# Optimization experiments

Hardware: AMD Instinct MI355X
Metric: run time of the kernel (lower is better)

Reference implementation:

```python
import jax, jax.numpy as jnp
import numpy as np

N = 100000      # nodes
E = 3200000     # edges (avg degree 32)
DU = 256        # unary_channels
DP = 256        # pairwise_channels (== out_channels, required by fusion cat)
H = 64          # hidden_channels = out_channels // 4
DO = 256        # out_channels
STEPS = 1
EPS = 1e-5      # BatchNorm eps (torch default)


def _bn(h, gamma, beta):
    # BatchNorm1d, training-mode batch stats (biased variance, as torch normalizes)
    mu = jnp.mean(h, axis=0)
    var = jnp.var(h, axis=0)
    return gamma * (h - mu) * jax.lax.rsqrt(var + EPS) + beta


def setup_inputs() -> dict:
    key = jax.random.key(0)
    ks = jax.random.split(key, 12)
    edge_index = jax.random.randint(ks[0], (2, E), 0, N, dtype=jnp.int64)
    return {
        "x": jax.random.normal(ks[1], (N, DU), dtype=jnp.float32),
        "y": jax.random.normal(ks[2], (N, DP), dtype=jnp.float32),
        "pos": jax.random.normal(ks[3], (N, 3), dtype=jnp.float32),
        "edge_index": edge_index,
        "Wu": jax.random.normal(ks[4], (DU, H), dtype=jnp.float32) / np.sqrt(DU),
        "gu": jnp.ones((H,), jnp.float32), "bu": jnp.zeros((H,), jnp.float32),
        "Wp": jax.random.normal(ks[5], (DP, H), dtype=jnp.float32) / np.sqrt(DP),
        "gp": jnp.ones((H,), jnp.float32), "bp": jnp.zeros((H,), jnp.float32),
        "c": jnp.eye(H, dtype=jnp.float32) + 0.1 * jax.random.normal(ks[6], (H, H), dtype=jnp.float32),
        "Wm": jax.random.normal(ks[7], (H, DO), dtype=jnp.float32) / np.sqrt(H),
        "gm": jnp.ones((DO,), jnp.float32), "bm": jnp.zeros((DO,), jnp.float32),
        "Wf": jax.random.normal(ks[8], (2 * DO, DO), dtype=jnp.float32) / np.sqrt(2 * DO),
        "gf": jnp.ones((DO,), jnp.float32), "bf": jnp.zeros((DO,), jnp.float32),
    }


def reference(x, y, pos, edge_index, Wu, gu, bu, Wp, gp, bp, c, Wm, gm, bm, Wf, gf, bf):
    i, j = edge_index[0], edge_index[1]
    # unary / pairwise embeddings (Linear no-bias + BN)
    xu = _bn(x @ Wu, gu, bu)                      # [N, H]
    su = _bn(y @ Wp, gp, bp)                      # [N, H]
    # edge logits: -||s_i - s_j||^2, softmax grouped by destination i
    d = su[i] - su[j]                             # [E, H]
    logit = -jnp.sum(d * d, axis=1, keepdims=True)  # [E, 1]
    m = jax.ops.segment_max(logit, i, num_segments=N)
    ex = jnp.exp(logit - m[i])
    denom = jax.ops.segment_sum(ex, i, num_segments=N)
    s = ex / (denom[i] + 1e-16)                   # [E, 1] edge softmax weights
    # CRF mean-field iterations with linear solve
    z = xu
    C = c.T @ c                                   # [H, H]
    Minv = jnp.linalg.inv(jnp.eye(H, dtype=x.dtype) + C)
    h = xu
    for _ in range(STEPS):
        agg = jax.ops.segment_sum(s * h[j], i, num_segments=N)  # gather-scale-scatter
        h = (z + agg @ C) @ Minv
    # output heads
    h = jax.nn.leaky_relu(_bn(h @ Wm, gm, bm))
    out = jax.nn.leaky_relu(_bn(jnp.concatenate([h, y], axis=-1) @ Wf, gf, bf))
    return out
```

## Files before the change

### kernel.cpp

```cpp
#include <hip/hip_runtime.h>
#include <hip/hip_fp16.h>
#include <math.h>

typedef unsigned short u16;
typedef short s16x8 __attribute__((ext_vector_type(8)));
typedef unsigned short u16x8 __attribute__((ext_vector_type(8)));
typedef float f32x4 __attribute__((ext_vector_type(4)));

__device__ __forceinline__ float bf2f(u16 u) {
  unsigned x = ((unsigned)u) << 16;
  return __uint_as_float(x);
}
__device__ __forceinline__ u16 f2bf(float f) {
  unsigned x = __float_as_uint(f);
  unsigned r = x + 0x7FFFu + ((x >> 16) & 1u);
  return (u16)(r >> 16);
}

static const size_t OFF_MINV   = 0;
static const size_t OFF_AU     = 32ull * 1024;
static const size_t OFF_BUE    = 32ull * 1024 + 256;
static const size_t OFF_AP     = 32ull * 1024 + 512;
static const size_t OFF_APBE   = 32ull * 1024 + 768;
static const size_t OFF_AM     = 36ull * 1024;
static const size_t OFF_BM     = 37ull * 1024;
static const size_t OFF_AF     = 38ull * 1024;
static const size_t OFF_BF     = 39ull * 1024;
static const size_t OFF_BTOT   = 40ull * 1024;
static const size_t OFF_BOFF   = 44ull * 1024;
static const size_t OFF_WUT    = 64ull * 1024;
static const size_t OFF_WMT    = 128ull * 1024;
static const size_t OFF_WFT    = 192ull * 1024;
static const size_t OFF_WPH    = 512ull * 1024;
static const size_t OFF_WPL    = 576ull * 1024;
static const size_t OFF_PART1  = 1ull  * 1024 * 1024;
static const size_t OFF_PART2  = 2ull  * 1024 * 1024;
static const size_t OFF_ROWPTR = 3ull  * 1024 * 1024;
static const size_t OFF_BLKCNT = 5ull  * 1024 * 1024;
static const size_t OFF_SRCJ   = 18ull * 1024 * 1024;
static const size_t OFF_U      = 44ull * 1024 * 1024;
static const size_t OFF_UN     = 57ull * 1024 * 1024;
static const size_t OFF_P      = 70ull * 1024 * 1024;
static const size_t OFF_PS     = 109ull * 1024 * 1024;
static const size_t OFF_H2     = 122ull * 1024 * 1024;

#define NBLK_BIN 1024

__global__ __launch_bounds__(256) void k_prep(const float* __restrict__ c,
                                              float* __restrict__ minv_out) {
  __shared__ float CC[4096];
  __shared__ float aug[64 * 129];
  __shared__ float fs[64];
  float* cl = aug;
  int t = threadIdx.x;
  for (int idx = t; idx < 4096; idx += 256) cl[idx] = c[idx];
  __syncthreads();
  for (int idx = t; idx < 4096; idx += 256) {
    int a = idx >> 6, b = idx & 63;
    float s = (a == b) ? 1.f : 0.f;
    for (int k = 0; k < 64; ++k) s += cl[k * 64 + a] * cl[k * 64 + b];
    CC[idx] = s;
  }
  __syncthreads();
  for (int idx = t; idx < 8192; idx += 256) {
    int r = idx >> 7, cc = idx & 127;
    aug[r * 129 + cc] = (cc < 64) ? CC[r * 64 + cc] : (((cc - 64) == r) ? 1.f : 0.f);
  }
  __syncthreads();
  int cloc = t & 127;
  int rbase = t >> 7;
  for (int p = 0; p < 64; ++p) {
    float inv = 1.0f / aug[p * 129 + p];
    if (t < 64) fs[t] = (t == p) ? 0.f : aug[t * 129 + p];
    __syncthreads();
    if (t < 128) aug[p * 129 + t] *= inv;
    __syncthreads();
    float pc = aug[p * 129 + cloc];
#pragma unroll
    for (int rr = 0; rr < 64; rr += 2) {
      int r = rr + rbase;
      aug[r * 129 + cloc] -= fs[r] * pc;
    }
    __syncthreads();
  }
  for (int idx = t; idx < 4096; idx += 256) {
    int r = idx >> 6, cc = idx & 63;
    minv_out[idx] = aug[r * 129 + 64 + cc];
  }
}

__global__ __launch_bounds__(256) void k_tcvt(const float* __restrict__ in, u16* __restrict__ outb,
                                              int Kd, int Nc) {
  int i = blockIdx.x * 256 + threadIdx.x;
  if (i < Kd * Nc) {
    int k = i / Nc, n = i - k * Nc;
    outb[(size_t)n * Kd + k] = f2bf(in[i]);
  }
}

__global__ __launch_bounds__(256) void k_tcvt_split(const float* __restrict__ in,
                                                    u16* __restrict__ outh, u16* __restrict__ outl) {
  int i = blockIdx.x * 256 + threadIdx.x;
  if (i < 256 * 64) {
    int k = i >> 6, n = i & 63;
    float v = in[i];
    u16 h = f2bf(v);
    float lo = v - bf2f(h);
    outh[(size_t)n * 256 + k] = h;
    outl[(size_t)n * 256 + k] = f2bf(lo);
  }
}

__global__ __launch_bounds__(256) void kA1(const int* __restrict__ ei, int E, int chunk,
                                           int* __restrict__ blockCnt, int nbk) {
  __shared__ int c[512];
  int t = threadIdx.x, bid = blockIdx.x;
  c[t] = 0; c[t + 256] = 0;
  __syncthreads();
  int e0 = bid * chunk, e1 = min(E, e0 + chunk);
  for (int e = e0 + t; e < e1; e += 256) atomicAdd(&c[ei[e] >> 8], 1);
  __syncthreads();
  for (int b = t; b < nbk; b += 256) blockCnt[(size_t)bid * nbk + b] = c[b];
}

__global__ __launch_bounds__(256) void kA2(int* __restrict__ blockCnt, int nbk,
                                           int* __restrict__ bucketTot) {
  int b = blockIdx.x, t = threadIdx.x;
  int base = t * 4;
  int v0 = blockCnt[(size_t)(base + 0) * nbk + b];
  int v1 = blockCnt[(size_t)(base + 1) * nbk + b];
  int v2 = blockCnt[(size_t)(base + 2) * nbk + b];
  int v3 = blockCnt[(size_t)(base + 3) * nbk + b];
  int s1 = v0 + v1, s2 = s1 + v2, tot = s2 + v3;
  __shared__ int ps[256];
  ps[t] = tot;
  __syncthreads();
  for (int off = 1; off < 256; off <<= 1) {
    int a = (t >= off) ? ps[t - off] : 0;
    __syncthreads();
    ps[t] += a;
    __syncthreads();
  }
  int ex = (t > 0) ? ps[t - 1] : 0;
  blockCnt[(size_t)(base + 0) * nbk + b] = ex;
  blockCnt[(size_t)(base + 1) * nbk + b] = ex + v0;
  blockCnt[(size_t)(base + 2) * nbk + b] = ex + s1;
  blockCnt[(size_t)(base + 3) * nbk + b] = ex + s2;
  if (t == 255) bucketTot[b] = ps[255];
}

__global__ __launch_bounds__(512) void kA2b(const int* __restrict__ bucketTot,
                                            int* __restrict__ bucketOff, int nbk) {
  __shared__ int s[512];
  int t = threadIdx.x;
  s[t] = (t < nbk) ? bucketTot[t] : 0;
  __syncthreads();
  for (int off = 1; off < 512; off <<= 1) {
    int a = (t >= off) ? s[t - off] : 0;
    __syncthreads();
    s[t] += a;
    __syncthreads();
  }
  if (t == 0) bucketOff[0] = 0;
  if (t < nbk) bucketOff[t + 1] = s[t];
}

__global__ __launch_bounds__(256) void kA3(const int* __restrict__ ei, const int* __restrict__ ej,
                                           int E, int chunk,
                                           const int* __restrict__ blockExc,
                                           const int* __restrict__ bucketOff,
                                           int nbk, uint2* __restrict__ tmp) {
  __shared__ int c[512], off[512], gb[512], cur[512];
  __shared__ uint2 stage[4096];
  int t = threadIdx.x, bid = blockIdx.x;
  c[t] = 0; c[t + 256] = 0;
  __syncthreads();
  int e0 = bid * chunk, e1 = min(E, e0 + chunk);
  int m = e1 - e0;
  for (int e = e0 + t; e < e1; e += 256) atomicAdd(&c[ei[e] >> 8], 1);
  __syncthreads();
  int v0 = c[t], v1 = c[t + 256];
  off[t] = v0; off[t + 256] = v1;
  __syncthreads();
  for (int o = 1; o < 512; o <<= 1) {
    int a0 = (t >= o) ? off[t - o] : 0;
    int a1 = ((t + 256) >= o) ? off[t + 256 - o] : 0;
    __syncthreads();
    off[t] += a0; off[t + 256] += a1;
    __syncthreads();
  }
  int ex0 = off[t] - v0, ex1 = off[t + 256] - v1;
  if (t < nbk)
    gb[t] = bucketOff[t] + blockExc[(size_t)bid * nbk + t] - ex0;
  if (t + 256 < nbk)
    gb[t + 256] = bucketOff[t + 256] + blockExc[(size_t)bid * nbk + t + 256] - ex1;
  cur[t] = ex0; cur[t + 256] = ex1;
  __syncthreads();
  for (int e = e0 + t; e < e1; e += 256) {
    int i = ei[e];
    int p = atomicAdd(&cur[i >> 8], 1);
    stage[p] = make_uint2((unsigned)i, (unsigned)ej[e]);
  }
  __syncthreads();
  for (int s = t; s < m; s += 256) {
    uint2 v = stage[s];
    tmp[gb[v.x >> 8] + s] = v;
  }
}

#define BCAP 12288
__global__ __launch_bounds__(256) void kB(const uint2* __restrict__ tmp,
                                          const int* __restrict__ bucketOff,
                                          int nbk, int N, int E,
                                          int* __restrict__ rowptr, int* __restrict__ srcj) {
  __shared__ int cnt[256], sc[256], cur[256];
  __shared__ int jbuf[BCAP];
  int b = blockIdx.x, t = threadIdx.x;
  int nb0 = b << 8;
  int e0 = bucketOff[b], e1 = bucketOff[b + 1];
  int m = e1 - e0;
  cnt[t] = 0;
  __syncthreads();
  for (int s = t; s < m; s += 256) atomicAdd(&cnt[tmp[e0 + s].x - nb0], 1);
  __syncthreads();
  int v = cnt[t];
  sc[t] = v;
  __syncthreads();
  for (int off = 1; off < 256; off <<= 1) {
    int a = (t >= off) ? sc[t - off] : 0;
    __syncthreads();
    sc[t] += a;
    __syncthreads();
  }
  int exc = sc[t] - v;
  cur[t] = exc;
  if (nb0 + t < N) rowptr[nb0 + t] = e0 + exc;
  if (b == nbk - 1 && t == 0) rowptr[N] = E;
  __syncthreads();
  for (int s = t; s < m; s += 256) {
    uint2 e = tmp[e0 + s];
    int p = atomicAdd(&cur[e.x - nb0], 1);
    if (p < BCAP) jbuf[p] = (int)e.y;
  }
  __syncthreads();
  for (int s = t; s < m; s += 256) srcj[e0 + s] = jbuf[s];
}

template<int BN, int AMODE, int OBF, int STATS>
__global__ __launch_bounds__(256) void k_mfma(const u16* __restrict__ Abf, const float* __restrict__ Af32,
                                              int ldA, int K, int M,
                                              const u16* __restrict__ h2, const float* __restrict__ yy,
                                              const float* __restrict__ am, const float* __restrict__ bm,
                                              const u16* __restrict__ Bt,
                                              float* __restrict__ Cf, u16* __restrict__ Cb, int ldC,
                                              int ncTot, float* __restrict__ p1, float* __restrict__ p2) {
  constexpr int WN  = BN / 2;
  constexpr int FN  = WN / 16;
  constexpr int NPB = BN / 32;
  __shared__ u16 lds[2][(128 + BN) * 64];

  int t = threadIdx.x;
  int wid = t >> 6, lane = t & 63;
  int wr = wid >> 1, wc = wid & 1;
  int lr = lane & 15, lk = lane >> 4;
  int m0 = blockIdx.x * 128;
  int n0 = blockIdx.y * BN;
  int nK = K >> 6;

  int sidx = t;
  u16x8 ra[4];
  u16x8 rb[NPB];

  f32x4 acc[4][FN];
#pragma unroll
  for (int m = 0; m < 4; ++m)
#pragma unroll
    for (int n = 0; n < FN; ++n) acc[m][n] = (f32x4){0.f, 0.f, 0.f, 0.f};

  auto loadTile = [&](int kk) {
    int kk0 = kk * 64;
#pragma unroll
    for (int p = 0; p < 4; ++p) {
      int idx = p * 256 + sidx;
      int r = idx >> 3, c8 = idx & 7;
      int row = m0 + r; if (row >= M) row = M - 1;
      int k = kk0 + c8 * 8;
      if constexpr (AMODE == 0) {
        ra[p] = *(const u16x8*)(Abf + (size_t)row * ldA + k);
      } else if constexpr (AMODE == 2) {
        const float* src = Af32 + (size_t)row * ldA + k;
        float4 a = *(const float4*)src;
        float4 b = *(const float4*)(src + 4);
        u16x8 o;
        o[0] = f2bf(a.x); o[1] = f2bf(a.y); o[2] = f2bf(a.z); o[3] = f2bf(a.w);
        o[4] = f2bf(b.x); o[5] = f2bf(b.y); o[6] = f2bf(b.z); o[7] = f2bf(b.w);
        ra[p] = o;
      } else {
        if (kk0 < 256) {
          u16x8 h8 = *(const u16x8*)(h2 + (size_t)row * 256 + k);
          float av[8], bv[8];
          *(float4*)(av)     = *(const float4*)(am + k);
          *(float4*)(av + 4) = *(const float4*)(am + k + 4);
          *(float4*)(bv)     = *(const float4*)(bm + k);
          *(float4*)(bv + 4) = *(const float4*)(bm + k + 4);
          u16x8 o;
#pragma unroll
          for (int j = 0; j < 8; ++j) {
            float v = bf2f((u16)h8[j]) * av[j] + bv[j];
            v = v > 0.f ? v : 0.01f * v;
            o[j] = f2bf(v);
          }
          ra[p] = o;
        } else {
          float yv[8];
          *(float4*)(yv)     = *(const float4*)(yy + (size_t)row * 256 + (k - 256));
          *(float4*)(yv + 4) = *(const float4*)(yy + (size_t)row * 256 + (k - 256) + 4);
          u16x8 o;
#pragma unroll
          for (int j = 0; j < 8; ++j) o[j] = f2bf(yv[j]);
          ra[p] = o;
        }
      }
    }
#pragma unroll
    for (int p = 0; p < NPB; ++p) {
      int idx = p * 256 + sidx;
      int r = idx >> 3, c8 = idx & 7;
      rb[p] = *(const u16x8*)(Bt + (size_t)(n0 + r) * K + kk0 + c8 * 8);
    }
  };

  auto dswrite = [&](int b) {
    char* As  = (char*)&lds[b][0];
    char* Bsc = As + 128 * 64 * 2;
#pragma unroll
    for (int p = 0; p < 4; ++p) {
      int idx = p * 256 + sidx;
      int r = idx >> 3, c8 = idx & 7;
      *(u16x8*)(As + r * 128 + ((c8 * 16) ^ ((r & 7) << 4))) = ra[p];
    }
#pragma unroll
    for (int p = 0; p < NPB; ++p) {
      int idx = p * 256 + sidx;
      int r = idx >> 3, c8 = idx & 7;
      *(u16x8*)(Bsc + r * 128 + ((c8 * 16) ^ ((r & 7) << 4))) = rb[p];
    }
  };

  auto compute = [&](int b) {
    const char* As  = (const char*)&lds[b][0];
    const char* Bsc = As + 128 * 64 * 2;
#pragma unroll
    for (int ks = 0; ks < 2; ++ks) {
      int kb = ks * 64 + lk * 16;
      s16x8 af[4], bfr[FN];
#pragma unroll
      for (int m = 0; m < 4; ++m) {
        int row = wr * 64 + m * 16 + lr;
        af[m] = *(const s16x8*)(As + row * 128 + (kb ^ ((row & 7) << 4)));
      }
#pragma unroll
      for (int n = 0; n < FN; ++n) {
        int row = wc * WN + n * 16 + lr;
        bfr[n] = *(const s16x8*)(Bsc + row * 128 + (kb ^ ((row & 7) << 4)));
      }
#pragma unroll
      for (int m = 0; m < 4; ++m)
#pragma unroll
        for (int n = 0; n < FN; ++n)
          acc[m][n] = __builtin_amdgcn_mfma_f32_16x16x32_bf16(af[m], bfr[n], acc[m][n], 0, 0, 0);
    }
  };

  loadTile(0);
  dswrite(0);
  __syncthreads();
  for (int kk = 0; kk < nK; ++kk) {
    int b = kk & 1;
    if (kk + 1 < nK) loadTile(kk + 1);
    compute(b);
    if (kk + 1 < nK) { dswrite(b ^ 1); __syncthreads(); }
  }

#pragma unroll
  for (int m = 0; m < 4; ++m) {
#pragma unroll
    for (int n = 0; n < FN; ++n) {
      int col = n0 + wc * WN + n * 16 + lr;
#pragma unroll
      for (int q = 0; q < 4; ++q) {
        int row = m0 + wr * 64 + m * 16 + lk * 4 + q;
        if (row < M) {
          if constexpr (OBF) Cb[(size_t)row * ldC + col] = f2bf(acc[m][n][q]);
          else               Cf[(size_t)row * ldC + col] = acc[m][n][q];
        }
      }
    }
  }

  if constexpr (STATS) {
    __syncthreads();
    float* sb = (float*)&lds[0][0];
#pragma unroll
    for (int n = 0; n < FN; ++n) {
      float s1 = 0.f, s2 = 0.f;
#pragma unroll
      for (int m = 0; m < 4; ++m)
#pragma unroll
        for (int q = 0; q < 4; ++q) {
          int row = m0 + wr * 64 + m * 16 + lk * 4 + q;
          float v = (row < M) ? acc[m][n][q] : 0.f;
          s1 += v; s2 += v * v;
        }
      s1 += __shfl_xor(s1, 16); s2 += __shfl_xor(s2, 16);
      s1 += __shfl_xor(s1, 32); s2 += __shfl_xor(s2, 32);
      if (lk == 0) {
        int c = wc * WN + n * 16 + lr;
        sb[(wr * BN + c) * 2 + 0] = s1;
        sb[(wr * BN + c) * 2 + 1] = s2;
      }
    }
    __syncthreads();
    if (t < BN) {
      float s1 = sb[t * 2]     + sb[(BN + t) * 2];
      float s2 = sb[t * 2 + 1] + sb[(BN + t) * 2 + 1];
      p1[(size_t)blockIdx.x * ncTot + n0 + t] = s1;
      p2[(size_t)blockIdx.x * ncTot + n0 + t] = s2;
    }
  }
}

__global__ __launch_bounds__(256) void k_mfma_split(const float* __restrict__ Af, int K, int M,
                                                    const u16* __restrict__ Bh, const u16* __restrict__ Bl,
                                                    float* __restrict__ Cf,
                                                    float* __restrict__ p1, float* __restrict__ p2) {
  __shared__ u16 sAh[128 * 64], sAl[128 * 64], sBh[64 * 64], sBl[64 * 64];
  int t = threadIdx.x;
  int wid = t >> 6, lane = t & 63;
  int wr = wid >> 1, wc = wid & 1;
  int lr = lane & 15, lk = lane >> 4;
  int m0 = blockIdx.x * 128;
  int nK = K >> 6;

  u16x8 rah[4], ral[4], rbh[2], rbl[2];
  f32x4 acc[4][2];
#pragma unroll
  for (int m = 0; m < 4; ++m)
#pragma unroll
    for (int n = 0; n < 2; ++n) acc[m][n] = (f32x4){0.f, 0.f, 0.f, 0.f};

  auto loadTile = [&](int kk) {
    int kk0 = kk * 64;
#pragma unroll
    for (int p = 0; p < 4; ++p) {
      int idx = p * 256 + t;
      int r = idx >> 3, c8 = idx & 7;
      int row = m0 + r; if (row >= M) row = M - 1;
      const float* src = Af + (size_t)row * K + kk0 + c8 * 8;
      float4 a = *(const float4*)src;
      float4 b = *(const float4*)(src + 4);
      float v[8];
      *(float4*)(v) = a; *(float4*)(v + 4) = b;
      u16x8 oh, ol;
#pragma unroll
      for (int j = 0; j < 8; ++j) {
        u16 h = f2bf(v[j]);
        oh[j] = h;
        ol[j] = f2bf(v[j] - bf2f(h));
      }
      rah[p] = oh; ral[p] = ol;
    }
#pragma unroll
    for (int p = 0; p < 2; ++p) {
      int idx = p * 256 + t;
      int r = idx >> 3, c8 = idx & 7;
      rbh[p] = *(const u16x8*)(Bh + (size_t)r * K + kk0 + c8 * 8);
      rbl[p] = *(const u16x8*)(Bl + (size_t)r * K + kk0 + c8 * 8);
    }
  };

  auto dswrite = [&]() {
    char* Ah = (char*)sAh; char* Al = (char*)sAl;
    char* Bhc = (char*)sBh; char* Blc = (char*)sBl;
#pragma unroll
    for (int p = 0; p < 4; ++p) {
      int idx = p * 256 + t;
      int r = idx >> 3, c8 = idx & 7;
      int off = r * 128 + ((c8 * 16) ^ ((r & 7) << 4));
      *(u16x8*)(Ah + off) = rah[p];
      *(u16x8*)(Al + off) = ral[p];
    }
#pragma unroll
    for (int p = 0; p < 2; ++p) {
      int idx = p * 256 + t;
      int r = idx >> 3, c8 = idx & 7;
      int off = r * 128 + ((c8 * 16) ^ ((r & 7) << 4));
      *(u16x8*)(Bhc + off) = rbh[p];
      *(u16x8*)(Blc + off) = rbl[p];
    }
  };

  auto compute = [&]() {
    const char* Ah = (const char*)sAh; const char* Al = (const char*)sAl;
    const char* Bhc = (const char*)sBh; const char* Blc = (const char*)sBl;
#pragma unroll
    for (int ks = 0; ks < 2; ++ks) {
      int kb = ks * 64 + lk * 16;
      s16x8 fah[4], fal[4], fbh[2], fbl[2];
#pragma unroll
      for (int m = 0; m < 4; ++m) {
        int row = wr * 64 + m * 16 + lr;
        int off = row * 128 + (kb ^ ((row & 7) << 4));
        fah[m] = *(const s16x8*)(Ah + off);
        fal[m] = *(const s16x8*)(Al + off);
      }
#pragma unroll
      for (int n = 0; n < 2; ++n) {
        int row = wc * 32 + n * 16 + lr;
        int off = row * 128 + (kb ^ ((row & 7) << 4));
        fbh[n] = *(const s16x8*)(Bhc + off);
        fbl[n] = *(const s16x8*)(Blc + off);
      }
#pragma unroll
      for (int m = 0; m < 4; ++m)
#pragma unroll
        for (int n = 0; n < 2; ++n) {
          acc[m][n] = __builtin_amdgcn_mfma_f32_16x16x32_bf16(fah[m], fbh[n], acc[m][n], 0, 0, 0);
          acc[m][n] = __builtin_amdgcn_mfma_f32_16x16x32_bf16(fah[m], fbl[n], acc[m][n], 0, 0, 0);
          acc[m][n] = __builtin_amdgcn_mfma_f32_16x16x32_bf16(fal[m], fbh[n], acc[m][n], 0, 0, 0);
        }
    }
  };

  loadTile(0);
  for (int kk = 0; kk < nK; ++kk) {
    __syncthreads();
    dswrite();
    __syncthreads();
    if (kk + 1 < nK) loadTile(kk + 1);
    compute();
  }

#pragma unroll
  for (int m = 0; m < 4; ++m) {
#pragma unroll
    for (int n = 0; n < 2; ++n) {
      int col = wc * 32 + n * 16 + lr;
#pragma unroll
      for (int q = 0; q < 4; ++q) {
        int row = m0 + wr * 64 + m * 16 + lk * 4 + q;
        if (row < M) Cf[(size_t)row * 64 + col] = acc[m][n][q];
      }
    }
  }

  __syncthreads();
  float* sb = (float*)sAh;
#pragma unroll
  for (int n = 0; n < 2; ++n) {
    float s1 = 0.f, s2 = 0.f;
#pragma unroll
    for (int m = 0; m < 4; ++m)
#pragma unroll
      for (int q = 0; q < 4; ++q) {
        int row = m0 + wr * 64 + m * 16 + lk * 4 + q;
        float v = (row < M) ? acc[m][n][q] : 0.f;
        s1 += v; s2 += v * v;
      }
    s1 += __shfl_xor(s1, 16); s2 += __shfl_xor(s2, 16);
    s1 += __shfl_xor(s1, 32); s2 += __shfl_xor(s2, 32);
    if (lk == 0) {
      int c = wc * 32 + n * 16 + lr;
      sb[(wr * 64 + c) * 2 + 0] = s1;
      sb[(wr * 64 + c) * 2 + 1] = s2;
    }
  }
  __syncthreads();
  if (t < 64) {
    float s1 = sb[t * 2]     + sb[(64 + t) * 2];
    float s2 = sb[t * 2 + 1] + sb[(64 + t) * 2 + 1];
    p1[(size_t)blockIdx.x * 64 + t] = s1;
    p2[(size_t)blockIdx.x * 64 + t] = s2;
  }
}

__global__ __launch_bounds__(256) void k_reduce_fin(const float* __restrict__ part1,
                                                    const float* __restrict__ part2,
                                                    int nb, int C, float invN,
                                                    const float* __restrict__ gamma,
                                                    const float* __restrict__ beta,
                                                    float* __restrict__ a_out,
                                                    float* __restrict__ b_out) {
  int c = blockIdx.x;
  int t = threadIdx.x;
  float s1 = 0.f, s2 = 0.f;
  for (int b = t; b < nb; b += 256) {
    s1 += part1[(size_t)b * C + c];
    s2 += part2[(size_t)b * C + c];
  }
  for (int m = 32; m; m >>= 1) { s1 += __shfl_xor(s1, m); s2 += __shfl_xor(s2, m); }
  __shared__ float l1[4], l2[4];
  if ((t & 63) == 0) { l1[t >> 6] = s1; l2[t >> 6] = s2; }
  __syncthreads();
  if (t == 0) {
    s1 = l1[0] + l1[1] + l1[2] + l1[3];
    s2 = l2[0] + l2[1] + l2[2] + l2[3];
    float mu  = s1 * invN;
    float var = s2 * invN - mu * mu;
    float a = gamma[c] * rsqrtf(var + 1e-5f);
    a_out[c] = a;
    b_out[c] = beta[c] - mu * a;
  }
}

__global__ __launch_bounds__(256) void k_scaleUN(const u16* __restrict__ ub, const float* __restrict__ au,
                                                 const float* __restrict__ bue, u16* __restrict__ un, int n8) {
  for (int i = blockIdx.x * 256 + threadIdx.x; i < n8; i += gridDim.x * 256) {
    int c0 = (i & 7) * 8;
    float av[8], bv[8];
    *(float4*)(av) = *(const float4*)(au + c0);  *(float4*)(av + 4) = *(const float4*)(au + c0 + 4);
    *(float4*)(bv) = *(const float4*)(bue + c0); *(float4*)(bv + 4) = *(const float4*)(bue + c0 + 4);
    u16x8 in = ((const u16x8*)ub)[i];
    u16x8 o;
#pragma unroll
    for (int j = 0; j < 8; ++j) o[j] = f2bf(bf2f((u16)in[j]) * av[j] + bv[j]);
    ((u16x8*)un)[i] = o;
  }
}

__global__ __launch_bounds__(256) void k_scaleP(const float* __restrict__ P, const float* __restrict__ ap,
                                                __half* __restrict__ PS, int n8) {
  for (int i = blockIdx.x * 256 + threadIdx.x; i < n8; i += gridDim.x * 256) {
    int c0 = (i & 7) * 8;
    float4 s0 = *(const float4*)(ap + c0), s1 = *(const float4*)(ap + c0 + 4);
    float4 a = ((const float4*)P)[i * 2];
    float4 b = ((const float4*)P)[i * 2 + 1];
    __half2 o0 = __floats2half2_rn(a.x * s0.x, a.y * s0.y);
    __half2 o1 = __floats2half2_rn(a.z * s0.z, a.w * s0.w);
    __half2 o2 = __floats2half2_rn(b.x * s1.x, b.y * s1.y);
    __half2 o3 = __floats2half2_rn(b.z * s1.z, b.w * s1.w);
    uint4 out;
    out.x = *(unsigned*)&o0; out.y = *(unsigned*)&o1;
    out.z = *(unsigned*)&o2; out.w = *(unsigned*)&o3;
    ((uint4*)PS)[i] = out;
  }
}

__global__ __launch_bounds__(256) void k_nodeall(const __half* __restrict__ PS,
                                                 const int* __restrict__ srcj,
                                                 const int* __restrict__ rowptr,
                                                 const u16* __restrict__ UN,
                                                 int N, float* __restrict__ agg) {
  int lane = threadIdx.x & 63;
  int node = blockIdx.x * 4 + (threadIdx.x >> 6);
  if (node >= N) return;
  int lane16 = lane & 15;
  int g4 = lane >> 4;
  const uint2* P2 = (const uint2*)PS;
  uint2 uu = P2[(size_t)node * 16 + lane16];
  float2 ua = __half22float2(*(const __half2*)&uu.x);
  float2 ub = __half22float2(*(const __half2*)&uu.y);
  float psl = __half2float(PS[(size_t)node * 64 + lane]);
  int b0 = rowptr[node], b1 = rowptr[node + 1];
  int deg = b1 - b0;
  float acc = 0.f;
  if (deg > 0) {
    int cnt = deg < 64 ? deg : 64;
    int jj = (lane < cnt) ? srcj[b0 + lane] : 0;
    float lg = -INFINITY;
    int capbase = lane & ~3;
    int capsrc  = (lane & 3) << 4;
    for (int ss = 0; ss < cnt; ss += 4) {
      int sl = ss + g4;
      int j = __shfl(jj, sl < cnt ? sl : cnt - 1);
      uint2 vv = P2[(size_t)j * 16 + lane16];
      float2 va = __half22float2(*(const __half2*)&vv.x);
      float2 vb = __half22float2(*(const __half2*)&vv.y);
      float d0 = ua.x - va.x, d1 = ua.y - va.y, d2 = ub.x - vb.x, d3 = ub.y - vb.y;
      float p = d0 * d0 + d1 * d1 + d2 * d2 + d3 * d3;
      p += __shfl_xor(p, 1, 16);
      p += __shfl_xor(p, 2, 16);
      p += __shfl_xor(p, 4, 16);
      p += __shfl_xor(p, 8, 16);
      float val = __shfl(p, capsrc);
      if (ss == capbase && lane < cnt) lg = -val;
    }
    float mx = lg;
    for (int s = b0 + 64; s < b1; ++s) {
      int j = srcj[s];
      float d = psl - __half2float(PS[(size_t)j * 64 + lane]);
      float p = d * d;
      for (int m = 32; m; m >>= 1) p += __shfl_xor(p, m);
      mx = fmaxf(mx, -p);
    }
    for (int m = 32; m; m >>= 1) mx = fmaxf(mx, __shfl_xor(mx, m));
    float ex = (lane < cnt) ? __expf(lg - mx) : 0.f;
    float sm = ex;
    for (int s = b0 + 64; s < b1; ++s) {
      int j = srcj[s];
      float d = psl - __half2float(PS[(size_t)j * 64 + lane]);
      float p = d * d;
      for (int m = 32; m; m >>= 1) p += __shfl_xor(p, m);
      if (lane == 0) sm += __expf(-p - mx);
    }
    for (int m = 32; m; m >>= 1) sm += __shfl_xor(sm, m);
    float inv = 1.0f / (sm + 1e-16f);
    float w = ex * inv;
    int ss = 0;
    for (; ss + 4 <= cnt; ss += 4) {
      int   j0 = __shfl(jj, ss),     j1 = __shfl(jj, ss + 1);
      int   j2 = __shfl(jj, ss + 2), j3 = __shfl(jj, ss + 3);
      float w0 = __shfl(w, ss),      w1 = __shfl(w, ss + 1);
      float w2 = __shfl(w, ss + 2),  w3 = __shfl(w, ss + 3);
      float v0 = bf2f(UN[(size_t)j0 * 64 + lane]);
      float v1 = bf2f(UN[(size_t)j1 * 64 + lane]);
      float v2 = bf2f(UN[(size_t)j2 * 64 + lane]);
      float v3 = bf2f(UN[(size_t)j3 * 64 + lane]);
      acc += w0 * v0 + w1 * v1 + w2 * v2 + w3 * v3;
    }
    for (; ss < cnt; ++ss) {
      int j0 = __shfl(jj, ss);
      float w0 = __shfl(w, ss);
      acc += w0 * bf2f(UN[(size_t)j0 * 64 + lane]);
    }
    for (int s = b0 + 64; s < b1; ++s) {
      int j = srcj[s];
      float d = psl - __half2float(PS[(size_t)j * 64 + lane]);
      float p = d * d;
      for (int m = 32; m; m >>= 1) p += __shfl_xor(p, m);
      acc += __expf(-p - mx) * inv * bf2f(UN[(size_t)j * 64 + lane]);
    }
  }
  agg[(size_t)node * 64 + lane] = acc;
}

__global__ __launch_bounds__(256) void k_solve(const u16* __restrict__ UN, const float* __restrict__ agg,
                                               const float* __restrict__ minv,
                                               u16* __restrict__ HB, int ntiles) {
  __shared__ float mS[4096];
  int t = threadIdx.x;
  int c16 = t & 15, rg = t >> 4;
  for (int idx = t; idx < 1024; idx += 256)
    ((float4*)mS)[idx] = ((const float4*)minv)[idx];
  __syncthreads();
  for (int tile = blockIdx.x; tile < ntiles; tile += gridDim.x) {
    int row = tile * 16 + rg;
    const u16*  ur = UN + (size_t)row * 64;
    const float* gr = agg + (size_t)row * 64;
    float4 acc = *(const float4*)(gr + c16 * 4);
#pragma unroll 4
    for (int k = 0; k < 64; ++k) {
      float z = bf2f(ur[k]) - gr[k];
      float4 m4 = ((const float4*)mS)[k * 16 + c16];
      acc.x += z * m4.x;
      acc.y += z * m4.y;
      acc.z += z * m4.z;
      acc.w += z * m4.w;
    }
    ((ushort4*)HB)[(size_t)row * 16 + c16] =
        make_ushort4(f2bf(acc.x), f2bf(acc.y), f2bf(acc.z), f2bf(acc.w));
  }
}

__global__ __launch_bounds__(256) void k_bnact16(const u16* __restrict__ raw, const float* __restrict__ af,
                                                 const float* __restrict__ bfp, float* __restrict__ out, int n8) {
  int i = blockIdx.x * 256 + threadIdx.x;
  int stride = gridDim.x * 256;
  for (; i < n8; i += stride) {
    int c0 = (i & 31) * 8;
    float av[8], bv[8];
    *(float4*)(av) = *(const float4*)(af + c0);  *(float4*)(av + 4) = *(const float4*)(af + c0 + 4);
    *(float4*)(bv) = *(const float4*)(bfp + c0); *(float4*)(bv + 4) = *(const float4*)(bfp + c0 + 4);
    u16x8 r = ((const u16x8*)raw)[i];
    float o[8];
#pragma unroll
    for (int j = 0; j < 8; ++j) {
      float v = bf2f((u16)r[j]) * av[j] + bv[j];
      o[j] = (v > 0.f) ? v : 0.01f * v;
    }
    ((float4*)out)[i * 2]     = *(float4*)(o);
    ((float4*)out)[i * 2 + 1] = *(float4*)(o + 4);
  }
}

extern "C" void kernel_launch(void* const* d_in, const int* in_sizes, int n_in,
                              void* d_out, int out_size, void* d_ws, size_t ws_size,
                              hipStream_t stream) {
  const float* x    = (const float*)d_in[0];
  const float* y    = (const float*)d_in[1];
  const int*   eidx = (const int*)d_in[3];
  const float* Wu   = (const float*)d_in[4];
  const float* gu   = (const float*)d_in[5];
  const float* bu   = (const float*)d_in[6];
  const float* Wp   = (const float*)d_in[7];
  const float* gp   = (const float*)d_in[8];
  const float* bp   = (const float*)d_in[9];
  const float* cIn  = (const float*)d_in[10];
  const float* Wm   = (const float*)d_in[11];
  const float* gm   = (const float*)d_in[12];
  const float* bm   = (const float*)d_in[13];
  const float* Wf   = (const float*)d_in[14];
  const float* gf   = (const float*)d_in[15];
  const float* bfv  = (const float*)d_in[16];

  const int N = in_sizes[0] / 256;
  const int E = in_sizes[3] / 2;
  const int* ei = eidx;
  const int* ej = eidx + E;

  char* ws = (char*)d_ws;
  float* MINV  = (float*)(ws + OFF_MINV);
  float* AU    = (float*)(ws + OFF_AU);
  float* BUE   = (float*)(ws + OFF_BUE);
  float* AP    = (float*)(ws + OFF_AP);
  float* APBE  = (float*)(ws + OFF_APBE);
  float* AM    = (float*)(ws + OFF_AM);
  float* BM    = (float*)(ws + OFF_BM);
  float* AF    = (float*)(ws + OFF_AF);
  float* BF    = (float*)(ws + OFF_BF);
  int*   BTOT  = (int*)(ws + OFF_BTOT);
  int*   BOFF  = (int*)(ws + OFF_BOFF);
  u16*   WUT   = (u16*)(ws + OFF_WUT);
  u16*   WMT   = (u16*)(ws + OFF_WMT);
  u16*   WFT   = (u16*)(ws + OFF_WFT);
  u16*   WPH   = (u16*)(ws + OFF_WPH);
  u16*   WPL   = (u16*)(ws + OFF_WPL);
  float* PART1 = (float*)(ws + OFF_PART1);
  float* PART2 = (float*)(ws + OFF_PART2);
  int*   ROWPTR= (int*)(ws + OFF_ROWPTR);
  int*   BLKCNT= (int*)(ws + OFF_BLKCNT);
  u16*   HB    = (u16*)(ws + OFF_BLKCNT);
  int*   SRCJ  = (int*)(ws + OFF_SRCJ);
  u16*   RAWO  = (u16*)(ws + OFF_SRCJ);
  u16*   UBRAW = (u16*)(ws + OFF_U);
  u16*   UN    = (u16*)(ws + OFF_UN);
  uint2* TMP   = (uint2*)(ws + OFF_P);
  float* P     = (float*)(ws + OFF_P);
  float* AGG   = (float*)(ws + OFF_P);
  __half* PS   = (__half*)(ws + OFF_PS);
  u16*   H2    = (u16*)(ws + OFF_H2);

  const float invN = 1.0f / (float)N;
  const int ntiles16 = N / 16;
  const int mtiles   = (N + 127) / 128;
  const int n8_64    = N * 64 / 8;
  const int n8_256   = N * 256 / 8;
  const int nbk      = (N + 255) >> 8;
  const int chunk    = (E + NBLK_BIN - 1) / NBLK_BIN;

  k_prep<<<1, 256, 0, stream>>>(cIn, MINV);
  k_tcvt<<<64,  256, 0, stream>>>(Wu, WUT, 256, 64);
  k_tcvt<<<64,  256, 0, stream>>>(Wm, WMT, 64, 256);
  k_tcvt<<<512, 256, 0, stream>>>(Wf, WFT, 512, 256);
  k_tcvt_split<<<64, 256, 0, stream>>>(Wp, WPH, WPL);

  kA1<<<NBLK_BIN, 256, 0, stream>>>(ei, E, chunk, BLKCNT, nbk);
  kA2<<<nbk, 256, 0, stream>>>(BLKCNT, nbk, BTOT);
  kA2b<<<1, 512, 0, stream>>>(BTOT, BOFF, nbk);
  kA3<<<NBLK_BIN, 256, 0, stream>>>(ei, ej, E, chunk, BLKCNT, BOFF, nbk, TMP);
  kB<<<nbk, 256, 0, stream>>>(TMP, BOFF, nbk, N, E, ROWPTR, SRCJ);

  k_mfma<64, 2, 1, 1><<<dim3(mtiles, 1), 256, 0, stream>>>(
      nullptr, x, 256, 256, N, nullptr, nullptr, nullptr, nullptr, WUT,
      nullptr, UBRAW, 64, 64, PART1, PART2);
  k_reduce_fin<<<64, 256, 0, stream>>>(PART1, PART2, mtiles, 64, invN, gu, bu, AU, BUE);
  k_scaleUN<<<1024, 256, 0, stream>>>(UBRAW, AU, BUE, UN, n8_64);

  k_mfma_split<<<mtiles, 256, 0, stream>>>(y, 256, N, WPH, WPL, P, PART1, PART2);
  k_reduce_fin<<<64, 256, 0, stream>>>(PART1, PART2, mtiles, 64, invN, gp, bp, AP, APBE);
  k_scaleP<<<1024, 256, 0, stream>>>(P, AP, PS, n8_64);

  k_nodeall<<<(N + 3) / 4, 256, 0, stream>>>(PS, SRCJ, ROWPTR, UN, N, AGG);

  k_solve<<<2048, 256, 0, stream>>>(UN, AGG, MINV, HB, ntiles16);

  k_mfma<128, 0, 1, 1><<<dim3(mtiles, 2), 256, 0, stream>>>(
      HB, nullptr, 64, 64, N, nullptr, nullptr, nullptr, nullptr, WMT,
      nullptr, H2, 256, 256, PART1, PART2);
  k_reduce_fin<<<256, 256, 0, stream>>>(PART1, PART2, mtiles, 256, invN, gm, bm, AM, BM);

  k_mfma<128, 1, 1, 1><<<dim3(mtiles, 2), 256, 0, stream>>>(
      nullptr, nullptr, 0, 512, N, H2, y, AM, BM, WFT,
      nullptr, RAWO, 256, 256, PART1, PART2);
  k_reduce_fin<<<256, 256, 0, stream>>>(PART1, PART2, mtiles, 256, invN, gf, bfv, AF, BF);
  k_bnact16<<<2048, 256, 0, stream>>>(RAWO, AF, BF, (float*)d_out, n8_256);
}
```

Baseline: 595.7 us.

## Fuse BN scaling and linear solve into edge aggregation; pack edge tmp to 32-bit

Removes the separate k_scaleUN pass and folds the unary BN affine into the aggregation: the weighted sum uses the raw values, then applies scale and shift once, which works because the softmax weights sum to one. It also fuses k_solve into k_nodeall through a per-wave shared-memory matrix-vector product. Other changes: the four weight-conversion kernels are merged into one launch, the bucket-sort temp buffer is packed into one 32-bit word per edge (8-bit local row plus 24-bit source), and the logit loop gathers 8 neighbours per step using 16-byte loads. The cost is that every node block now loads the 16KB Minv into shared memory, and it adds more register and LDS pressure in the fused kernel.

```diff
diff --git a/kernel.cpp b/kernel.cpp
--- a/kernel.cpp
+++ b/kernel.cpp
@@ -39,7 +39,6 @@
 static const size_t OFF_BLKCNT = 5ull  * 1024 * 1024;
 static const size_t OFF_SRCJ   = 18ull * 1024 * 1024;
 static const size_t OFF_U      = 44ull * 1024 * 1024;
-static const size_t OFF_UN     = 57ull * 1024 * 1024;
 static const size_t OFF_P      = 70ull * 1024 * 1024;
 static const size_t OFF_PS     = 109ull * 1024 * 1024;
 static const size_t OFF_H2     = 122ull * 1024 * 1024;
@@ -89,25 +88,31 @@
   }
 }
 
-__global__ __launch_bounds__(256) void k_tcvt(const float* __restrict__ in, u16* __restrict__ outb,
-                                              int Kd, int Nc) {
-  int i = blockIdx.x * 256 + threadIdx.x;
-  if (i < Kd * Nc) {
-    int k = i / Nc, n = i - k * Nc;
-    outb[(size_t)n * Kd + k] = f2bf(in[i]);
-  }
-}
-
-__global__ __launch_bounds__(256) void k_tcvt_split(const float* __restrict__ in,
-                                                    u16* __restrict__ outh, u16* __restrict__ outl) {
-  int i = blockIdx.x * 256 + threadIdx.x;
-  if (i < 256 * 64) {
+__global__ __launch_bounds__(256) void k_tcvt_all(const float* __restrict__ Wu, const float* __restrict__ Wm,
+                                                  const float* __restrict__ Wf, const float* __restrict__ Wp,
+                                                  u16* __restrict__ WUT, u16* __restrict__ WMT,
+                                                  u16* __restrict__ WFT, u16* __restrict__ WPH,
+                                                  u16* __restrict__ WPL) {
+  int b = blockIdx.x, t = threadIdx.x;
+  if (b < 64) {
+    int i = b * 256 + t;
     int k = i >> 6, n = i & 63;
-    float v = in[i];
+    WUT[(size_t)n * 256 + k] = f2bf(Wu[i]);
+  } else if (b < 128) {
+    int i = (b - 64) * 256 + t;
+    int k = i >> 8, n = i & 255;
+    WMT[(size_t)n * 64 + k] = f2bf(Wm[i]);
+  } else if (b < 640) {
+    int i = (b - 128) * 256 + t;
+    int k = i >> 8, n = i & 255;
+    WFT[(size_t)n * 512 + k] = f2bf(Wf[i]);
+  } else {
+    int i = (b - 640) * 256 + t;
+    int k = i >> 6, n = i & 63;
+    float v = Wp[i];
     u16 h = f2bf(v);
-    float lo = v - bf2f(h);
-    outh[(size_t)n * 256 + k] = h;
-    outl[(size_t)n * 256 + k] = f2bf(lo);
+    WPH[(size_t)n * 256 + k] = h;
+    WPL[(size_t)n * 256 + k] = f2bf(v - bf2f(h));
   }
 }
 
@@ -169,7 +174,7 @@
                                            int E, int chunk,
                                            const int* __restrict__ blockExc,
                                            const int* __restrict__ bucketOff,
-                                           int nbk, uint2* __restrict__ tmp) {
+                                           int nbk, unsigned* __restrict__ tmp) {
   __shared__ int c[512], off[512], gb[512], cur[512];
   __shared__ uint2 stage[4096];
   int t = threadIdx.x, bid = blockIdx.x;
@@ -204,12 +209,12 @@
   __syncthreads();
   for (int s = t; s < m; s += 256) {
     uint2 v = stage[s];
-    tmp[gb[v.x >> 8] + s] = v;
+    tmp[gb[v.x >> 8] + s] = ((v.x & 255u) << 24) | v.y;
   }
 }
 
 #define BCAP 12288
-__global__ __launch_bounds__(256) void kB(const uint2* __restrict__ tmp,
+__global__ __launch_bounds__(256) void kB(const unsigned* __restrict__ tmp,
                                           const int* __restrict__ bucketOff,
                                           int nbk, int N, int E,
                                           int* __restrict__ rowptr, int* __restrict__ srcj) {
@@ -221,7 +226,7 @@
   int m = e1 - e0;
   cnt[t] = 0;
   __syncthreads();
-  for (int s = t; s < m; s += 256) atomicAdd(&cnt[tmp[e0 + s].x - nb0], 1);
+  for (int s = t; s < m; s += 256) atomicAdd(&cnt[tmp[e0 + s] >> 24], 1);
   __syncthreads();
   int v = cnt[t];
   sc[t] = v;
@@ -238,9 +243,9 @@
   if (b == nbk - 1 && t == 0) rowptr[N] = E;
   __syncthreads();
   for (int s = t; s < m; s += 256) {
-    uint2 e = tmp[e0 + s];
-    int p = atomicAdd(&cur[e.x - nb0], 1);
-    if (p < BCAP) jbuf[p] = (int)e.y;
+    unsigned e = tmp[e0 + s];
+    int p = atomicAdd(&cur[e >> 24], 1);
+    if (p < BCAP) jbuf[p] = (int)(e & 0xFFFFFFu);
   }
   __syncthreads();
   for (int s = t; s < m; s += 256) srcj[e0 + s] = jbuf[s];
@@ -613,21 +618,6 @@
   }
 }
 
-__global__ __launch_bounds__(256) void k_scaleUN(const u16* __restrict__ ub, const float* __restrict__ au,
-                                                 const float* __restrict__ bue, u16* __restrict__ un, int n8) {
-  for (int i = blockIdx.x * 256 + threadIdx.x; i < n8; i += gridDim.x * 256) {
-    int c0 = (i & 7) * 8;
-    float av[8], bv[8];
-    *(float4*)(av) = *(const float4*)(au + c0);  *(float4*)(av + 4) = *(const float4*)(au + c0 + 4);
-    *(float4*)(bv) = *(const float4*)(bue + c0); *(float4*)(bv + 4) = *(const float4*)(bue + c0 + 4);
-    u16x8 in = ((const u16x8*)ub)[i];
-    u16x8 o;
-#pragma unroll
-    for (int j = 0; j < 8; ++j) o[j] = f2bf(bf2f((u16)in[j]) * av[j] + bv[j]);
-    ((u16x8*)un)[i] = o;
-  }
-}
-
 __global__ __launch_bounds__(256) void k_scaleP(const float* __restrict__ P, const float* __restrict__ ap,
                                                 __half* __restrict__ PS, int n8) {
   for (int i = blockIdx.x * 256 + threadIdx.x; i < n8; i += gridDim.x * 256) {
@@ -649,39 +639,55 @@
 __global__ __launch_bounds__(256) void k_nodeall(const __half* __restrict__ PS,
                                                  const int* __restrict__ srcj,
                                                  const int* __restrict__ rowptr,
-                                                 const u16* __restrict__ UN,
-                                                 int N, float* __restrict__ agg) {
-  int lane = threadIdx.x & 63;
-  int node = blockIdx.x * 4 + (threadIdx.x >> 6);
+                                                 const u16* __restrict__ UB,
+                                                 const float* __restrict__ au,
+                                                 const float* __restrict__ bue,
+                                                 const float* __restrict__ minv,
+                                                 int N, u16* __restrict__ HB) {
+  __shared__ float mS[4096];
+  __shared__ float zma[4][64];
+  int t = threadIdx.x;
+  for (int idx = t; idx < 1024; idx += 256)
+    ((float4*)mS)[idx] = ((const float4*)minv)[idx];
+  __syncthreads();
+
+  int lane = t & 63, wid = t >> 6;
+  int node = blockIdx.x * 4 + wid;
   if (node >= N) return;
-  int lane16 = lane & 15;
-  int g4 = lane >> 4;
-  const uint2* P2 = (const uint2*)PS;
-  uint2 uu = P2[(size_t)node * 16 + lane16];
-  float2 ua = __half22float2(*(const __half2*)&uu.x);
-  float2 ub = __half22float2(*(const __half2*)&uu.y);
+
+  int lane8 = lane & 7, g8 = lane >> 3;
+  const uint4* P4 = (const uint4*)PS;
+  uint4 uv = P4[(size_t)node * 8 + lane8];
+  float2 u0 = __half22float2(*(const __half2*)&uv.x);
+  float2 u1 = __half22float2(((const __half2*)&uv.x)[1]);
+  float2 u2 = __half22float2(*(const __half2*)&uv.z);
+  float2 u3 = __half22float2(((const __half2*)&uv.z)[1]);
   float psl = __half2float(PS[(size_t)node * 64 + lane]);
   int b0 = rowptr[node], b1 = rowptr[node + 1];
   int deg = b1 - b0;
-  float acc = 0.f;
+  float aggv = 0.f;
   if (deg > 0) {
     int cnt = deg < 64 ? deg : 64;
     int jj = (lane < cnt) ? srcj[b0 + lane] : 0;
     float lg = -INFINITY;
-    int capbase = lane & ~3;
-    int capsrc  = (lane & 3) << 4;
-    for (int ss = 0; ss < cnt; ss += 4) {
-      int sl = ss + g4;
-      int j = __shfl(jj, sl < cnt ? sl : cnt - 1);
-      uint2 vv = P2[(size_t)j * 16 + lane16];
-      float2 va = __half22float2(*(const __half2*)&vv.x);
-      float2 vb = __half22float2(*(const __half2*)&vv.y);
-      float d0 = ua.x - va.x, d1 = ua.y - va.y, d2 = ub.x - vb.x, d3 = ub.y - vb.y;
-      float p = d0 * d0 + d1 * d1 + d2 * d2 + d3 * d3;
-      p += __shfl_xor(p, 1, 16);
-      p += __shfl_xor(p, 2, 16);
-      p += __shfl_xor(p, 4, 16);
-      p += __shfl_xor(p, 8, 16);
+    int capbase = lane & ~7;
+    int capsrc  = (lane & 7) << 3;
+    for (int ss = 0; ss < cnt; ss += 8) {
+      int sl = ss + g8; if (sl >= cnt) sl = cnt - 1;
+      int j = __shfl(jj, sl);
+      uint4 vv = P4[(size_t)j * 8 + lane8];
+      float2 v0 = __half22float2(*(const __half2*)&vv.x);
+      float2 v1 = __half22float2(((const __half2*)&vv.x)[1]);
+      float2 v2 = __half22float2(*(const __half2*)&vv.z);
+      float2 v3 = __half22float2(((const __half2*)&vv.z)[1]);
+      float d0 = u0.x - v0.x, d1 = u0.y - v0.y;
+      float d2 = u1.x - v1.x, d3 = u1.y - v1.y;
+      float d4 = u2.x - v2.x, d5 = u2.y - v2.y;
+      float d6 = u3.x - v3.x, d7 = u3.y - v3.y;
+      float p = d0*d0 + d1*d1 + d2*d2 + d3*d3 + d4*d4 + d5*d5 + d6*d6 + d7*d7;
+      p += __shfl_xor(p, 1, 8);
+      p += __shfl_xor(p, 2, 8);
+      p += __shfl_xor(p, 4, 8);
       float val = __shfl(p, capsrc);
       if (ss == capbase && lane < cnt) lg = -val;
     }
@@ -706,60 +712,48 @@
     for (int m = 32; m; m >>= 1) sm += __shfl_xor(sm, m);
     float inv = 1.0f / (sm + 1e-16f);
     float w = ex * inv;
+    float acc = 0.f;
     int ss = 0;
-    for (; ss + 4 <= cnt; ss += 4) {
+    for (; ss + 8 <= cnt; ss += 8) {
       int   j0 = __shfl(jj, ss),     j1 = __shfl(jj, ss + 1);
       int   j2 = __shfl(jj, ss + 2), j3 = __shfl(jj, ss + 3);
+      int   j4 = __shfl(jj, ss + 4), j5 = __shfl(jj, ss + 5);
+      int   j6 = __shfl(jj, ss + 6), j7 = __shfl(jj, ss + 7);
       float w0 = __shfl(w, ss),      w1 = __shfl(w, ss + 1);
       float w2 = __shfl(w, ss + 2),  w3 = __shfl(w, ss + 3);
-      float v0 = bf2f(UN[(size_t)j0 * 64 + lane]);
-      float v1 = bf2f(UN[(size_t)j1 * 64 + lane]);
-      float v2 = bf2f(UN[(size_t)j2 * 64 + lane]);
-      float v3 = bf2f(UN[(size_t)j3 * 64 + lane]);
+      float w4 = __shfl(w, ss + 4),  w5 = __shfl(w, ss + 5);
+      float w6 = __shfl(w, ss + 6),  w7 = __shfl(w, ss + 7);
+      float v0 = bf2f(UB[(size_t)j0 * 64 + lane]);
+      float v1 = bf2f(UB[(size_t)j1 * 64 + lane]);
+      float v2 = bf2f(UB[(size_t)j2 * 64 + lane]);
+      float v3 = bf2f(UB[(size_t)j3 * 64 + lane]);
+      float v4 = bf2f(UB[(size_t)j4 * 64 + lane]);
+      float v5 = bf2f(UB[(size_t)j5 * 64 + lane]);
+      float v6 = bf2f(UB[(size_t)j6 * 64 + lane]);
+      float v7 = bf2f(UB[(size_t)j7 * 64 + lane]);
       acc += w0 * v0 + w1 * v1 + w2 * v2 + w3 * v3;
+      acc += w4 * v4 + w5 * v5 + w6 * v6 + w7 * v7;
     }
     for (; ss < cnt; ++ss) {
       int j0 = __shfl(jj, ss);
       float w0 = __shfl(w, ss);
-      acc += w0 * bf2f(UN[(size_t)j0 * 64 + lane]);
+      acc += w0 * bf2f(UB[(size_t)j0 * 64 + lane]);
     }
     for (int s = b0 + 64; s < b1; ++s) {
       int j = srcj[s];
       float d = psl - __half2float(PS[(size_t)j * 64 + lane]);
       float p = d * d;
       for (int m = 32; m; m >>= 1) p += __shfl_xor(p, m);
-      acc += __expf(-p - mx) * inv * bf2f(UN[(size_t)j * 64 + lane]);
-    }
-  }
-  agg[(size_t)node * 64 + lane] = acc;
-}
-
-__global__ __launch_bounds__(256) void k_solve(const u16* __restrict__ UN, const float* __restrict__ agg,
-                                               const float* __restrict__ minv,
-                                               u16* __restrict__ HB, int ntiles) {
-  __shared__ float mS[4096];
-  int t = threadIdx.x;
-  int c16 = t & 15, rg = t >> 4;
-  for (int idx = t; idx < 1024; idx += 256)
-    ((float4*)mS)[idx] = ((const float4*)minv)[idx];
-  __syncthreads();
-  for (int tile = blockIdx.x; tile < ntiles; tile += gridDim.x) {
-    int row = tile * 16 + rg;
-    const u16*  ur = UN + (size_t)row * 64;
-    const float* gr = agg + (size_t)row * 64;
-    float4 acc = *(const float4*)(gr + c16 * 4);
-#pragma unroll 4
-    for (int k = 0; k < 64; ++k) {
-      float z = bf2f(ur[k]) - gr[k];
-      float4 m4 = ((const float4*)mS)[k * 16 + c16];
-      acc.x += z * m4.x;
-      acc.y += z * m4.y;
-      acc.z += z * m4.z;
-      acc.w += z * m4.w;
-    }
-    ((ushort4*)HB)[(size_t)row * 16 + c16] =
-        make_ushort4(f2bf(acc.x), f2bf(acc.y), f2bf(acc.z), f2bf(acc.w));
-  }
+      acc += __expf(-p - mx) * inv * bf2f(UB[(size_t)j * 64 + lane]);
+    }
+    aggv = au[lane] * acc + bue[lane];
+  }
+  float z = au[lane] * bf2f(UB[(size_t)node * 64 + lane]) + bue[lane];
+  zma[wid][lane] = z - aggv;
+  float h = aggv;
+#pragma unroll 8
+  for (int k = 0; k < 64; ++k) h += zma[wid][k] * mS[k * 64 + lane];
+  HB[(size_t)node * 64 + lane] = f2bf(h);
 }
 
 __global__ __launch_bounds__(256) void k_bnact16(const u16* __restrict__ raw, const float* __restrict__ af,
@@ -833,15 +827,12 @@
   int*   SRCJ  = (int*)(ws + OFF_SRCJ);
   u16*   RAWO  = (u16*)(ws + OFF_SRCJ);
   u16*   UBRAW = (u16*)(ws + OFF_U);
-  u16*   UN    = (u16*)(ws + OFF_UN);
-  uint2* TMP   = (uint2*)(ws + OFF_P);
+  unsigned* TMP= (unsigned*)(ws + OFF_P);
   float* P     = (float*)(ws + OFF_P);
-  float* AGG   = (float*)(ws + OFF_P);
   __half* PS   = (__half*)(ws + OFF_PS);
   u16*   H2    = (u16*)(ws + OFF_H2);
 
   const float invN = 1.0f / (float)N;
-  const int ntiles16 = N / 16;
   const int mtiles   = (N + 127) / 128;
   const int n8_64    = N * 64 / 8;
   const int n8_256   = N * 256 / 8;
@@ -849,10 +840,7 @@
   const int chunk    = (E + NBLK_BIN - 1) / NBLK_BIN;
 
   k_prep<<<1, 256, 0, stream>>>(cIn, MINV);
-  k_tcvt<<<64,  256, 0, stream>>>(Wu, WUT, 256, 64);
-  k_tcvt<<<64,  256, 0, stream>>>(Wm, WMT, 64, 256);
-  k_tcvt<<<512, 256, 0, stream>>>(Wf, WFT, 512, 256);
-  k_tcvt_split<<<64, 256, 0, stream>>>(Wp, WPH, WPL);
+  k_tcvt_all<<<704, 256, 0, stream>>>(Wu, Wm, Wf, Wp, WUT, WMT, WFT, WPH, WPL);
 
   kA1<<<NBLK_BIN, 256, 0, stream>>>(ei, E, chunk, BLKCNT, nbk);
   kA2<<<nbk, 256, 0, stream>>>(BLKCNT, nbk, BTOT);
@@ -864,15 +852,12 @@
       nullptr, x, 256, 256, N, nullptr, nullptr, nullptr, nullptr, WUT,
       nullptr, UBRAW, 64, 64, PART1, PART2);
   k_reduce_fin<<<64, 256, 0, stream>>>(PART1, PART2, mtiles, 64, invN, gu, bu, AU, BUE);
-  k_scaleUN<<<1024, 256, 0, stream>>>(UBRAW, AU, BUE, UN, n8_64);
 
   k_mfma_split<<<mtiles, 256, 0, stream>>>(y, 256, N, WPH, WPL, P, PART1, PART2);
   k_reduce_fin<<<64, 256, 0, stream>>>(PART1, PART2, mtiles, 64, invN, gp, bp, AP, APBE);
   k_scaleP<<<1024, 256, 0, stream>>>(P, AP, PS, n8_64);
 
-  k_nodeall<<<(N + 3) / 4, 256, 0, stream>>>(PS, SRCJ, ROWPTR, UN, N, AGG);
-
-  k_solve<<<2048, 256, 0, stream>>>(UN, AGG, MINV, HB, ntiles16);
+  k_nodeall<<<(N + 3) / 4, 256, 0, stream>>>(PS, SRCJ, ROWPTR, UBRAW, AU, BUE, MINV, N, HB);
 
   k_mfma<128, 0, 1, 1><<<dim3(mtiles, 2), 256, 0, stream>>>(
       HB, nullptr, 64, 64, N, nullptr, nullptr, nullptr, nullptr, WMT,
```

New measurement: 550.5 us. 1.08x faster.
